# Kernel optimization log

Measured on AMD Instinct MI355X. Metric: run time of the kernel, lower is better.

The kernel has to match this reference:

```python
import jax, jax.numpy as jnp
import numpy as np

N, E, DIN, H, C, ED = 50000, 500000, 264, 4, 32, 16
HID = H * C   # 128
OUT = 128
NEG_SLOPE = 0.2
LN_EPS = 1e-5


def _ln(x, g, b):
    mu = jnp.mean(x, axis=-1, keepdims=True)
    var = jnp.mean((x - mu) ** 2, axis=-1, keepdims=True)
    return (x - mu) * jax.lax.rsqrt(var + LN_EPS) * g + b


def _segment_softmax(scores, seg, num_segments):
    # scores: (E, H), seg: (E,) destination node ids
    m = jax.ops.segment_max(scores, seg, num_segments=num_segments)
    m = jnp.where(jnp.isfinite(m), m, 0.0)
    ex = jnp.exp(scores - m[seg])
    s = jax.ops.segment_sum(ex, seg, num_segments=num_segments)
    return ex / (s[seg] + 1e-16)


def _gatv2(x, src, dst, edge_attr, Wl, bl, Wr, br, We, att, bias):
    # GATv2Conv (PyG semantics): lin_l -> source, lin_r -> target, lin_edge (no bias)
    n = x.shape[0]
    xl = (x @ Wl + bl).reshape(n, H, C)          # source transform
    xr = (x @ Wr + br).reshape(n, H, C)          # target transform
    ee = (edge_attr @ We).reshape(-1, H, C)      # (E, H, C)
    m = xl[src] + xr[dst] + ee                   # per-edge pre-activation
    g = jnp.where(m > 0, m, NEG_SLOPE * m)       # leaky_relu(0.2)
    score = jnp.einsum('ehc,hc->eh', g, att)     # (E, H)
    alpha = _segment_softmax(score, dst, n)      # softmax over in-edges of each dst
    msg = xl[src] * alpha[..., None]             # (E, H, C)
    out = jax.ops.segment_sum(msg, dst, num_segments=n)
    return out.reshape(n, HID) + bias


def setup_inputs() -> dict:
    key = jax.random.key(0)
    ks = jax.random.split(key, 16)
    r = lambda k, s: jax.random.normal(k, s, dtype=jnp.float32) * 0.05
    return {
        'x': jax.random.normal(ks[0], (N, DIN), jnp.float32),
        'edge_attr': jax.random.normal(ks[1], (E, ED), jnp.float32),
        'Wl1': r(ks[2], (DIN, HID)), 'bl1': jnp.zeros((HID,), jnp.float32),
        'Wr1': r(ks[3], (DIN, HID)), 'br1': jnp.zeros((HID,), jnp.float32),
        'We1': r(ks[4], (ED, HID)), 'att1': r(ks[5], (H, C)), 'bias1': jnp.zeros((HID,), jnp.float32),
        'Wl2': r(ks[6], (HID, HID)), 'bl2': jnp.zeros((HID,), jnp.float32),
        'Wr2': r(ks[7], (HID, HID)), 'br2': jnp.zeros((HID,), jnp.float32),
        'We2': r(ks[8], (ED, HID)), 'att2': r(ks[9], (H, C)), 'bias2': jnp.zeros((HID,), jnp.float32),
        'Wres': r(ks[10], (DIN, HID)), 'bres': jnp.zeros((HID,), jnp.float32),
        'Wout': r(ks[11], (HID, OUT)), 'bout': jnp.zeros((OUT,), jnp.float32),
        'g1': jnp.ones((HID,), jnp.float32), 'bn1': jnp.zeros((HID,), jnp.float32),
        'g2': jnp.ones((HID,), jnp.float32), 'bn2': jnp.zeros((HID,), jnp.float32),
        'go': jnp.ones((OUT,), jnp.float32), 'bo': jnp.zeros((OUT,), jnp.float32),
        'edge_index': jax.random.randint(ks[12], (2, E), 0, N, dtype=jnp.int32),
    }


def reference(x, edge_attr, Wl1, bl1, Wr1, br1, We1, att1, bias1,
              Wl2, bl2, Wr2, br2, We2, att2, bias2,
              Wres, bres, Wout, bout, g1, bn1, g2, bn2, go, bo, edge_index):
    src, dst = edge_index[0], edge_index[1]
    residual = x @ Wres + bres
    h = _gatv2(x, src, dst, edge_attr, Wl1, bl1, Wr1, br1, We1, att1, bias1)
    h = jax.nn.elu(h)
    h = _ln(h + residual, g1, bn1)
    residual = h
    h = _gatv2(h, src, dst, edge_attr, Wl2, bl2, Wr2, br2, We2, att2, bias2)
    h = jax.nn.elu(h)
    h = _ln(h + residual, g2, bn2)
    context = _ln(h @ Wout + bout, go, bo)
    return context
```

## Files before the change

kernel.cpp:

```cpp
#include <hip/hip_runtime.h>
#include <hip/hip_bf16.h>
#include <math.h>
#include <stdint.h>

#define NN 50000
#define NE 500000
#define DIN 264
#define KP1 288
#define HID 128
#define EDIM 16

typedef __attribute__((ext_vector_type(8))) short short8;
typedef __attribute__((ext_vector_type(4))) float f32x4;

__device__ __forceinline__ short f2bf(float v) {
    union { float f; unsigned u; } x; x.f = v;
    unsigned r = x.u + 0x7fff + ((x.u >> 16) & 1);
    return (short)(r >> 16);
}
__device__ __forceinline__ float bf2f(short v) {
    union { float f; unsigned u; } x;
    x.u = ((unsigned)(unsigned short)v) << 16;
    return x.f;
}
__device__ __forceinline__ float bflo(unsigned u) {
    union { float f; unsigned u; } x; x.u = u << 16; return x.f;
}
__device__ __forceinline__ float bfhi(unsigned u) {
    union { float f; unsigned u; } x; x.u = u & 0xffff0000u; return x.f;
}
__device__ __forceinline__ unsigned pk2bf(float a, float b) {
    return (unsigned)(unsigned short)f2bf(a) | ((unsigned)(unsigned short)f2bf(b) << 16);
}

__device__ __forceinline__ void gload_lds16(const void* g, void* l) {
    __builtin_amdgcn_global_load_lds(
        (const __attribute__((address_space(1))) unsigned int*)g,
        (__attribute__((address_space(3))) unsigned int*)l, 16, 0, 0);
}

__global__ void k_count(const int* __restrict__ dst, int* __restrict__ cnt) {
    int e = blockIdx.x * blockDim.x + threadIdx.x;
    if (e < NE) atomicAdd(&cnt[dst[e]], 1);
}

__global__ __launch_bounds__(256) void k_scan1(const int* __restrict__ cnt,
                                               int* __restrict__ off, int* __restrict__ bsum) {
    __shared__ int buf[256];
    int b = blockIdx.x, t = threadIdx.x;
    int i = b * 256 + t;
    int v = (i < NN) ? cnt[i] : 0;
    buf[t] = v; __syncthreads();
    for (int s = 1; s < 256; s <<= 1) {
        int u = (t >= s) ? buf[t - s] : 0; __syncthreads();
        buf[t] += u; __syncthreads();
    }
    if (i < NN) off[i + 1] = buf[t];
    if (t == 255) bsum[b] = buf[255];
}

__global__ void k_scan2(int* __restrict__ bsum, int nb) {
    __shared__ int buf[256];
    int t = threadIdx.x;
    int o = (t < nb) ? bsum[t] : 0;
    buf[t] = o; __syncthreads();
    for (int s = 1; s < 256; s <<= 1) {
        int u = (t >= s) ? buf[t - s] : 0; __syncthreads();
        buf[t] += u; __syncthreads();
    }
    if (t < nb) bsum[t] = buf[t] - o;
}

__global__ void k_scan3c(int* __restrict__ off, const int* __restrict__ bsum,
                         int* __restrict__ cur) {
    int j = blockIdx.x * 256 + threadIdx.x;
    if (j > NN) return;
    int v = (j == 0) ? 0 : off[j] + bsum[(j - 1) >> 8];
    off[j] = v;
    if (j < NN) cur[j] = v;
}

__global__ void k_scatter(const int* __restrict__ src, const int* __restrict__ dst,
                          int* __restrict__ cur, int* __restrict__ srcp,
                          int* __restrict__ dstp, int* __restrict__ ey) {
    int e = blockIdx.x * blockDim.x + threadIdx.x;
    if (e < NE) {
        int d = dst[e];
        int p = atomicAdd(&cur[d], 1);
        srcp[p] = src[e];
        dstp[p] = d;
        ey[p] = e;
    }
}

__global__ void k_cvt_x(const float* __restrict__ x, short* __restrict__ xb) {
    int idx = blockIdx.x * 256 + threadIdx.x;
    if (idx >= NN * KP1) return;
    int i = idx / KP1, k = idx - i * KP1;
    xb[idx] = (k < DIN) ? f2bf(x[(size_t)i * DIN + k]) : (short)0;
}

__global__ void k_prep_w(const float* __restrict__ Wl1, const float* __restrict__ Wr1,
                         const float* __restrict__ Wres, const float* __restrict__ Wl2,
                         const float* __restrict__ Wr2, const float* __restrict__ Wout,
                         const float* __restrict__ bl1, const float* __restrict__ br1,
                         const float* __restrict__ bres, const float* __restrict__ bl2,
                         const float* __restrict__ br2,
                         const float* __restrict__ We1, const float* __restrict__ We2,
                         const float* __restrict__ att1, const float* __restrict__ att2,
                         short* __restrict__ Wt1, short* __restrict__ Wt2,
                         short* __restrict__ Wt3, float* __restrict__ bcat1,
                         float* __restrict__ bcat2,
                         short* __restrict__ WeT1, short* __restrict__ WeT2,
                         short* __restrict__ attB1, short* __restrict__ attB2) {
    int idx = blockIdx.x * 256 + threadIdx.x;
    if (idx < 384 * KP1) {
        int n = idx / KP1, k = idx - n * KP1;
        float v = 0.f;
        if (k < DIN) {
            const float* W = (n < 128) ? Wl1 : ((n < 256) ? Wr1 : Wres);
            v = W[(size_t)k * 128 + (n & 127)];
        }
        Wt1[idx] = f2bf(v);
        return;
    }
    idx -= 384 * KP1;
    if (idx < 256 * 128) {
        int n = idx >> 7, k = idx & 127;
        const float* W = (n < 128) ? Wl2 : Wr2;
        Wt2[idx] = f2bf(W[(size_t)k * 128 + (n & 127)]);
        return;
    }
    idx -= 256 * 128;
    if (idx < 128 * 128) {
        int n = idx >> 7, k = idx & 127;
        Wt3[idx] = f2bf(Wout[(size_t)k * 128 + n]);
        return;
    }
    idx -= 128 * 128;
    if (idx < 384) {
        bcat1[idx] = (idx < 128) ? bl1[idx] : ((idx < 256) ? br1[idx - 128] : bres[idx - 256]);
        return;
    }
    idx -= 384;
    if (idx < 256) {
        bcat2[idx] = (idx < 128) ? bl2[idx] : br2[idx - 128];
        return;
    }
    idx -= 256;
    if (idx < 128 * 32) {
        int n = idx >> 5, k = idx & 31;
        WeT1[idx] = (k < EDIM) ? f2bf(We1[(size_t)k * 128 + n]) : (short)0;
        return;
    }
    idx -= 128 * 32;
    if (idx < 128 * 32) {
        int n = idx >> 5, k = idx & 31;
        WeT2[idx] = (k < EDIM) ? f2bf(We2[(size_t)k * 128 + n]) : (short)0;
        return;
    }
    idx -= 128 * 32;
    if (idx < 16 * 128) {
        int n = idx >> 7, k = idx & 127;
        attB1[idx] = (n == (k >> 5)) ? f2bf(att1[k]) : (short)0;
        return;
    }
    idx -= 16 * 128;
    if (idx < 16 * 128) {
        int n = idx >> 7, k = idx & 127;
        attB2[idx] = (n == (k >> 5)) ? f2bf(att2[k]) : (short)0;
    }
}

__global__ __launch_bounds__(256) void k_gather_ea(const int* __restrict__ ey,
                                                   const float* __restrict__ ea,
                                                   short* __restrict__ eaperm) {
    int pos = blockIdx.x * 256 + threadIdx.x;
    if (pos >= NE) return;
    int e = ey[pos];
    const float4* r = (const float4*)(ea + (size_t)e * EDIM);
    float4 v0 = r[0], v1 = r[1], v2 = r[2], v3 = r[3];
    uint4 w0 = make_uint4(pk2bf(v0.x, v0.y), pk2bf(v0.z, v0.w),
                          pk2bf(v1.x, v1.y), pk2bf(v1.z, v1.w));
    uint4 w1 = make_uint4(pk2bf(v2.x, v2.y), pk2bf(v2.z, v2.w),
                          pk2bf(v3.x, v3.y), pk2bf(v3.z, v3.w));
    uint4* o = (uint4*)(eaperm + (size_t)pos * 32);
    o[0] = w0; o[1] = w1;
    o[2] = make_uint4(0, 0, 0, 0);
    o[3] = make_uint4(0, 0, 0, 0);
}

template <bool BF16OUT>
__global__ __launch_bounds__(256) void k_mfma_gemm(const short* __restrict__ A,
                                                   const short* __restrict__ Bt,
                                                   const float* __restrict__ bias,
                                                   float* __restrict__ Cf,
                                                   short* __restrict__ Cb,
                                                   int M, int Kpad, int NS) {
    __shared__ short As[128 * 32];
    __shared__ short Bs[128 * 32];
    int t = threadIdx.x;
    int lane = t & 63, wid = t >> 6;
    int wm = (wid & 1) * 64, wn = (wid >> 1) * 64;
    int cl = lane & 15, quad = lane >> 4;
    int row0 = blockIdx.x * 128;
    int col0 = blockIdx.y * 128;

    f32x4 acc[4][4];
#pragma unroll
    for (int i = 0; i < 4; ++i)
#pragma unroll
        for (int j = 0; j < 4; ++j) acc[i][j] = (f32x4)0.f;

    for (int k0 = 0; k0 < Kpad; k0 += 32) {
#pragma unroll
        for (int r = 0; r < 2; ++r) {
            int c = t + r * 256;
            int m = c >> 2;
            int row = row0 + m; if (row >= M) row = M - 1;
            const char* ga = (const char*)A + ((size_t)row * Kpad + k0) * 2 + (c & 3) * 16;
            gload_lds16(ga, (char*)As + c * 16);
            int n = col0 + m;
            const char* gb = (const char*)Bt + ((size_t)n * Kpad + k0) * 2 + (c & 3) * 16;
            gload_lds16(gb, (char*)Bs + c * 16);
        }
        __syncthreads();

        short8 a[4], b[4];
#pragma unroll
        for (int mi = 0; mi < 4; ++mi)
            a[mi] = *(const short8*)&As[(wm + mi * 16 + cl) * 32 + quad * 8];
#pragma unroll
        for (int ni = 0; ni < 4; ++ni)
            b[ni] = *(const short8*)&Bs[(wn + ni * 16 + cl) * 32 + quad * 8];
#pragma unroll
        for (int mi = 0; mi < 4; ++mi)
#pragma unroll
            for (int ni = 0; ni < 4; ++ni)
                acc[mi][ni] = __builtin_amdgcn_mfma_f32_16x16x32_bf16(a[mi], b[ni], acc[mi][ni], 0, 0, 0);
        __syncthreads();
    }

#pragma unroll
    for (int mi = 0; mi < 4; ++mi)
#pragma unroll
        for (int ni = 0; ni < 4; ++ni) {
            int col = col0 + wn + ni * 16 + cl;
            float bv = bias[col];
#pragma unroll
            for (int r = 0; r < 4; ++r) {
                int row = row0 + wm + mi * 16 + quad * 4 + r;
                if (row < M) {
                    float v = acc[mi][ni][r] + bv;
                    if (BF16OUT) Cb[(size_t)row * NS + col] = f2bf(v);
                    else         Cf[(size_t)row * NS + col] = v;
                }
            }
        }
}

__global__ __launch_bounds__(256) void k_gemm_ln(const short* __restrict__ A,
                                                 const short* __restrict__ Bt,
                                                 const float* __restrict__ bias,
                                                 const float* __restrict__ gamma,
                                                 const float* __restrict__ beta,
                                                 float* __restrict__ out, int M) {
    __shared__ short As[128 * 32];
    __shared__ short Bs[128 * 32];
    __shared__ float redS[128][2];
    int t = threadIdx.x;
    int lane = t & 63, wid = t >> 6;
    int wm = (wid & 1) * 64, wn = (wid >> 1) * 64;
    int cl = lane & 15, quad = lane >> 4;
    int row0 = blockIdx.x * 128;
    int wh = wid >> 1;

    f32x4 acc[4][4];
#pragma unroll
    for (int i = 0; i < 4; ++i)
#pragma unroll
        for (int j = 0; j < 4; ++j) acc[i][j] = (f32x4)0.f;

    for (int k0 = 0; k0 < 128; k0 += 32) {
#pragma unroll
        for (int r = 0; r < 2; ++r) {
            int c = t + r * 256;
            int m = c >> 2;
            int row = row0 + m; if (row >= M) row = M - 1;
            const char* ga = (const char*)A + ((size_t)row * 128 + k0) * 2 + (c & 3) * 16;
            gload_lds16(ga, (char*)As + c * 16);
            const char* gb = (const char*)Bt + ((size_t)m * 128 + k0) * 2 + (c & 3) * 16;
            gload_lds16(gb, (char*)Bs + c * 16);
        }
        __syncthreads();

        short8 a[4], b[4];
#pragma unroll
        for (int mi = 0; mi < 4; ++mi)
            a[mi] = *(const short8*)&As[(wm + mi * 16 + cl) * 32 + quad * 8];
#pragma unroll
        for (int ni = 0; ni < 4; ++ni)
            b[ni] = *(const short8*)&Bs[(wn + ni * 16 + cl) * 32 + quad * 8];
#pragma unroll
        for (int mi = 0; mi < 4; ++mi)
#pragma unroll
            for (int ni = 0; ni < 4; ++ni)
                acc[mi][ni] = __builtin_amdgcn_mfma_f32_16x16x32_bf16(a[mi], b[ni], acc[mi][ni], 0, 0, 0);
        __syncthreads();
    }

    float bv[4], gv[4], bev[4];
#pragma unroll
    for (int ni = 0; ni < 4; ++ni) {
        int col = wn + ni * 16 + cl;
        bv[ni] = bias[col]; gv[ni] = gamma[col]; bev[ni] = beta[col];
    }

    float s[4][4];
#pragma unroll
    for (int mi = 0; mi < 4; ++mi)
#pragma unroll
        for (int r = 0; r < 4; ++r) {
            float v = (acc[mi][0][r] + bv[0]) + (acc[mi][1][r] + bv[1]) +
                      (acc[mi][2][r] + bv[2]) + (acc[mi][3][r] + bv[3]);
            v += __shfl_xor(v, 1, 64);
            v += __shfl_xor(v, 2, 64);
            v += __shfl_xor(v, 4, 64);
            v += __shfl_xor(v, 8, 64);
            s[mi][r] = v;
        }
    if (cl == 0) {
#pragma unroll
        for (int mi = 0; mi < 4; ++mi)
#pragma unroll
            for (int r = 0; r < 4; ++r)
                redS[wm + mi * 16 + quad * 4 + r][wh] = s[mi][r];
    }
    __syncthreads();
    float mean[4][4];
#pragma unroll
    for (int mi = 0; mi < 4; ++mi)
#pragma unroll
        for (int r = 0; r < 4; ++r) {
            int rl = wm + mi * 16 + quad * 4 + r;
            mean[mi][r] = (redS[rl][0] + redS[rl][1]) * (1.f / 128.f);
        }
    __syncthreads();

#pragma unroll
    for (int mi = 0; mi < 4; ++mi)
#pragma unroll
        for (int r = 0; r < 4; ++r) {
            float q = 0.f;
#pragma unroll
            for (int ni = 0; ni < 4; ++ni) {
                float d = acc[mi][ni][r] + bv[ni] - mean[mi][r];
                q = fmaf(d, d, q);
            }
            q += __shfl_xor(q, 1, 64);
            q += __shfl_xor(q, 2, 64);
            q += __shfl_xor(q, 4, 64);
            q += __shfl_xor(q, 8, 64);
            s[mi][r] = q;
        }
    if (cl == 0) {
#pragma unroll
        for (int mi = 0; mi < 4; ++mi)
#pragma unroll
            for (int r = 0; r < 4; ++r)
                redS[wm + mi * 16 + quad * 4 + r][wh] = s[mi][r];
    }
    __syncthreads();

#pragma unroll
    for (int mi = 0; mi < 4; ++mi)
#pragma unroll
        for (int r = 0; r < 4; ++r) {
            int rl = wm + mi * 16 + quad * 4 + r;
            int row = row0 + rl;
            if (row < M) {
                float rstd = rsqrtf((redS[rl][0] + redS[rl][1]) * (1.f / 128.f) + 1e-5f);
#pragma unroll
                for (int ni = 0; ni < 4; ++ni) {
                    int col = wn + ni * 16 + cl;
                    float d = acc[mi][ni][r] + bv[ni] - mean[mi][r];
                    out[(size_t)row * 128 + col] = fmaf(d * rstd, gv[ni], bev[ni]);
                }
            }
        }
}

template <int STRIDE>
__global__ __launch_bounds__(512) void k_edge_score(const short* __restrict__ eaperm,
                                                    const short* __restrict__ WeT,
                                                    const short* __restrict__ attB,
                                                    const int* __restrict__ srcp,
                                                    const int* __restrict__ dstp,
                                                    const short* __restrict__ C,
                                                    float* __restrict__ pe) {
    __shared__ short Gs[128 * 136];
    __shared__ short Ab[16 * 136];
    __shared__ int sS[128], sD[128];
    int t = threadIdx.x;
    int lane = t & 63, wid = t >> 6;
    int wm2 = (wid & 1) * 64;
    int wn2 = (wid >> 1) * 32;
    int cl = lane & 15, quad = lane >> 4;
    long e0 = (long)blockIdx.x * 128;

    if (t < 128) {
        long ep = e0 + t; if (ep >= NE) ep = NE - 1;
        sS[t] = srcp[ep];
        sD[t] = dstp[ep];
    } else if (t < 384) {
        int u = t - 128;
        int rr = u >> 4, cc = (u & 15) * 8;
        *(short8*)&Ab[rr * 136 + cc] = *(const short8*)&attB[rr * 128 + cc];
    }

    short8 a[4], b[2];
#pragma unroll
    for (int mi = 0; mi < 4; ++mi) {
        long e = e0 + wm2 + mi * 16 + cl; if (e >= NE) e = NE - 1;
        a[mi] = *(const short8*)&eaperm[e * 32 + quad * 8];
    }
#pragma unroll
    for (int ni = 0; ni < 2; ++ni)
        b[ni] = *(const short8*)&WeT[(size_t)(wn2 + ni * 16 + cl) * 32 + quad * 8];

    f32x4 acc[4][2];
#pragma unroll
    for (int i = 0; i < 4; ++i) { acc[i][0] = (f32x4)0.f; acc[i][1] = (f32x4)0.f; }
#pragma unroll
    for (int mi = 0; mi < 4; ++mi)
#pragma unroll
        for (int ni = 0; ni < 2; ++ni)
            acc[mi][ni] = __builtin_amdgcn_mfma_f32_16x16x32_bf16(a[mi], b[ni], acc[mi][ni], 0, 0, 0);
    __syncthreads();

#pragma unroll
    for (int mi = 0; mi < 4; ++mi) {
#pragma unroll
        for (int r = 0; r < 4; ++r) {
            int eloc = wm2 + mi * 16 + quad * 4 + r;
            const short* xlr = C + (size_t)sS[eloc] * STRIDE;
            const short* xrr = C + (size_t)sD[eloc] * STRIDE + 128;
            int f0 = wn2 + cl, f1 = wn2 + 16 + cl;
            float xl0 = bf2f(xlr[f0]), xr0 = bf2f(xrr[f0]);
            float xl1 = bf2f(xlr[f1]), xr1 = bf2f(xrr[f1]);
            float g0 = acc[mi][0][r] + xl0 + xr0;
            float g1 = acc[mi][1][r] + xl1 + xr1;
            g0 = fmaxf(g0, 0.2f * g0);
            g1 = fmaxf(g1, 0.2f * g1);
            Gs[eloc * 136 + f0] = f2bf(g0);
            Gs[eloc * 136 + f1] = f2bf(g1);
        }
    }
    __syncthreads();

    f32x4 sacc = (f32x4)0.f;
    int em0 = wid * 16;
#pragma unroll
    for (int ks = 0; ks < 4; ++ks) {
        short8 ag = *(const short8*)&Gs[(em0 + cl) * 136 + ks * 32 + quad * 8];
        short8 bg = *(const short8*)&Ab[cl * 136 + ks * 32 + quad * 8];
        sacc = __builtin_amdgcn_mfma_f32_16x16x32_bf16(ag, bg, sacc, 0, 0, 0);
    }

    if (cl < 4) {
#pragma unroll
        for (int r = 0; r < 4; ++r) {
            long epos = e0 + em0 + quad * 4 + r;
            if (epos < NE) pe[epos * 4 + cl] = __expf(sacc[r]);
        }
    }
}

template <int STRIDE>
__global__ __launch_bounds__(256) void k_fused_agg(const int* __restrict__ off,
                                                   const int* __restrict__ srcp,
                                                   const float* __restrict__ pe,
                                                   const short* __restrict__ C,
                                                   const short* __restrict__ resid, int rstride,
                                                   const float* __restrict__ bias,
                                                   const float* __restrict__ gamma,
                                                   const float* __restrict__ beta,
                                                   short* __restrict__ outb) {
    int t = threadIdx.x;
    int w = t >> 6, l = t & 63;
    int f0 = (l >> 4) * 32 + (l & 15) * 2;
    int fp = f0 >> 1;
    int hd = l >> 4;

    float2 bs2 = ((const float2*)bias)[fp];
    float2 gv = ((const float2*)gamma)[fp];
    float2 bev = ((const float2*)beta)[fp];

    int n0 = (blockIdx.x * 4 + w) * 4;
    int nend = n0 + 4; if (nend > NN) nend = NN;

    for (int i = n0; i < nend; ++i) {
        unsigned rp = *(const unsigned*)&resid[(size_t)i * rstride + f0];
        int b0 = off[i], b1 = off[i + 1];

        float lA = 0.f, aA0 = 0.f, aA1 = 0.f;
        float lB = 0.f, aB0 = 0.f, aB1 = 0.f;
        int pos = b0;
        int sA = 0, sB = 0; float pA = 0.f, pB = 0.f;
        bool have = (pos + 2 <= b1);
        if (have) {
            sA = srcp[pos]; sB = srcp[pos + 1];
            pA = pe[(size_t)pos * 4 + hd]; pB = pe[(size_t)(pos + 1) * 4 + hd];
        }
        while (have) {
            bool haven = (pos + 4 <= b1);
            int nsA = 0, nsB = 0; float npA = 0.f, npB = 0.f;
            if (haven) {
                nsA = srcp[pos + 2]; nsB = srcp[pos + 3];
                npA = pe[(size_t)(pos + 2) * 4 + hd]; npB = pe[(size_t)(pos + 3) * 4 + hd];
            }
            unsigned xlA = *(const unsigned*)&C[(size_t)sA * STRIDE + f0];
            unsigned xlB = *(const unsigned*)&C[(size_t)sB * STRIDE + f0];
            lA += pA; lB += pB;
            aA0 = fmaf(pA, bflo(xlA), aA0);
            aA1 = fmaf(pA, bfhi(xlA), aA1);
            aB0 = fmaf(pB, bflo(xlB), aB0);
            aB1 = fmaf(pB, bfhi(xlB), aB1);
            pos += 2;
            sA = nsA; sB = nsB; pA = npA; pB = npB;
            have = haven;
        }
        if (pos < b1) {
            int s1 = srcp[pos];
            float p1 = pe[(size_t)pos * 4 + hd];
            unsigned xlv = *(const unsigned*)&C[(size_t)s1 * STRIDE + f0];
            lA += p1;
            aA0 = fmaf(p1, bflo(xlv), aA0);
            aA1 = fmaf(p1, bfhi(xlv), aA1);
        }
        float l_run = lA + lB;
        float acc0 = aA0 + aB0, acc1 = aA1 + aB1;

        float inv = 1.f / (l_run + 1e-16f);
        float o0 = fmaf(acc0, inv, bs2.x);
        float o1 = fmaf(acc1, inv, bs2.y);
        o0 = o0 > 0.f ? o0 : (__expf(o0) - 1.f);
        o1 = o1 > 0.f ? o1 : (__expf(o1) - 1.f);
        float v0 = o0 + bflo(rp), v1 = o1 + bfhi(rp);
        float s = v0 + v1;
#pragma unroll
        for (int o = 32; o > 0; o >>= 1) s += __shfl_xor(s, o, 64);
        float mean = s * (1.f / 128.f);
        float d0 = v0 - mean, d1 = v1 - mean;
        float q = fmaf(d0, d0, d1 * d1);
#pragma unroll
        for (int o = 32; o > 0; o >>= 1) q += __shfl_xor(q, o, 64);
        float rstd = rsqrtf(q * (1.f / 128.f) + 1e-5f);
        float r0 = fmaf(d0 * rstd, gv.x, bev.x);
        float r1 = fmaf(d1 * rstd, gv.y, bev.y);
        unsigned op = (unsigned)(unsigned short)f2bf(r0) |
                      (((unsigned)(unsigned short)f2bf(r1)) << 16);
        *(unsigned*)&outb[(size_t)i * 128 + f0] = op;
    }
}

extern "C" void kernel_launch(void* const* d_in, const int* in_sizes, int n_in,
                              void* d_out, int out_size, void* d_ws, size_t ws_size,
                              hipStream_t stream) {
    (void)in_sizes; (void)n_in; (void)out_size; (void)ws_size;
    const float* x     = (const float*)d_in[0];
    const float* ea    = (const float*)d_in[1];
    const float* Wl1   = (const float*)d_in[2];
    const float* bl1   = (const float*)d_in[3];
    const float* Wr1   = (const float*)d_in[4];
    const float* br1   = (const float*)d_in[5];
    const float* We1   = (const float*)d_in[6];
    const float* att1  = (const float*)d_in[7];
    const float* bias1 = (const float*)d_in[8];
    const float* Wl2   = (const float*)d_in[9];
    const float* bl2   = (const float*)d_in[10];
    const float* Wr2   = (const float*)d_in[11];
    const float* br2   = (const float*)d_in[12];
    const float* We2   = (const float*)d_in[13];
    const float* att2  = (const float*)d_in[14];
    const float* bias2 = (const float*)d_in[15];
    const float* Wres  = (const float*)d_in[16];
    const float* bres  = (const float*)d_in[17];
    const float* Wout  = (const float*)d_in[18];
    const float* bout  = (const float*)d_in[19];
    const float* g1    = (const float*)d_in[20];
    const float* bn1   = (const float*)d_in[21];
    const float* g2    = (const float*)d_in[22];
    const float* bn2   = (const float*)d_in[23];
    const float* go    = (const float*)d_in[24];
    const float* bo    = (const float*)d_in[25];
    const int*   ei    = (const int*)d_in[26];
    const int* srcv = ei;
    const int* dstv = ei + NE;
    float* outp = (float*)d_out;

    char* p = (char*)d_ws;
    auto carve = [&](size_t bytes) {
        char* r = p;
        p += (bytes + 255) & ~(size_t)255;
        return r;
    };
    short* xb    = (short*)carve((size_t)NN * KP1 * 2);
    short* Wt1   = (short*)carve((size_t)384 * KP1 * 2);
    short* Wt2   = (short*)carve((size_t)256 * 128 * 2);
    short* Wt3   = (short*)carve((size_t)128 * 128 * 2);
    short* WeT1  = (short*)carve((size_t)128 * 32 * 2);
    short* WeT2  = (short*)carve((size_t)128 * 32 * 2);
    short* attB1 = (short*)carve((size_t)16 * 128 * 2);
    short* attB2 = (short*)carve((size_t)16 * 128 * 2);
    float* bcat1 = (float*)carve(384 * 4);
    float* bcat2 = (float*)carve(256 * 4);
    short* C1    = (short*)carve((size_t)NN * 384 * 2);
    short* h1b   = (short*)carve((size_t)NN * 128 * 2);
    short* h2b   = (short*)carve((size_t)NN * 128 * 2);
    int* off     = (int*)carve((size_t)(NN + 1) * 4);
    int* cur     = (int*)carve((size_t)NN * 4);
    int* bsum    = (int*)carve(256 * 4);
    int* srcp    = (int*)carve((size_t)NE * 4);
    int* dstp    = (int*)carve((size_t)NE * 4);
    int* ey      = (int*)carve((size_t)NE * 4);
    short* eaperm = (short*)carve((size_t)NE * 32 * 2);
    float* pe    = (float*)carve((size_t)NE * 4 * 4);

    short* C2 = C1;

    const int NB = (NN + 255) / 256;

    hipMemsetAsync(cur, 0, (size_t)NN * 4, stream);
    k_count<<<(NE + 255) / 256, 256, 0, stream>>>(dstv, cur);
    k_scan1<<<NB, 256, 0, stream>>>(cur, off, bsum);
    k_scan2<<<1, 256, 0, stream>>>(bsum, NB);
    k_scan3c<<<(NN + 256) / 256, 256, 0, stream>>>(off, bsum, cur);
    k_scatter<<<(NE + 255) / 256, 256, 0, stream>>>(srcv, dstv, cur, srcp, dstp, ey);

    k_cvt_x<<<((size_t)NN * KP1 + 255) / 256, 256, 0, stream>>>(x, xb);
    int prep_total = 384 * KP1 + 256 * 128 + 128 * 128 + 384 + 256 + 2 * 128 * 32 + 2 * 16 * 128;
    k_prep_w<<<(prep_total + 255) / 256, 256, 0, stream>>>(Wl1, Wr1, Wres, Wl2, Wr2, Wout,
                                                           bl1, br1, bres, bl2, br2,
                                                           We1, We2, att1, att2,
                                                           Wt1, Wt2, Wt3, bcat1, bcat2,
                                                           WeT1, WeT2, attB1, attB2);
    k_gather_ea<<<(NE + 255) / 256, 256, 0, stream>>>(ey, ea, eaperm);

    int mb  = (NN + 127) / 128;
    int ebk = (NE + 127) / 128;
    int gagg = (NN + 15) / 16;

    k_mfma_gemm<true><<<dim3(mb, 3), 256, 0, stream>>>(xb, Wt1, bcat1, nullptr, C1, NN, KP1, 384);
    k_edge_score<384><<<ebk, 512, 0, stream>>>(eaperm, WeT1, attB1, srcp, dstp, C1, pe);
    k_fused_agg<384><<<gagg, 256, 0, stream>>>(off, srcp, pe, C1,
                                               C1 + 256, 384, bias1, g1, bn1, h1b);
    k_mfma_gemm<true><<<dim3(mb, 2), 256, 0, stream>>>(h1b, Wt2, bcat2, nullptr, C2, NN, 128, 256);
    k_edge_score<256><<<ebk, 512, 0, stream>>>(eaperm, WeT2, attB2, srcp, dstp, C2, pe);
    k_fused_agg<256><<<gagg, 256, 0, stream>>>(off, srcp, pe, C2,
                                               h1b, 128, bias2, g2, bn2, h2b);
    k_gemm_ln<<<mb, 256, 0, stream>>>(h2b, Wt3, bout, go, bo, outp, NN);
}
```

Before: 483.8 us.

## Drop permuted edge-attr buffer; gather and convert edge attributes inside edge-score kernel

```diff
diff --git a/kernel.cpp b/kernel.cpp
--- a/kernel.cpp
+++ b/kernel.cpp
@@ -28,9 +28,6 @@
 }
 __device__ __forceinline__ float bfhi(unsigned u) {
     union { float f; unsigned u; } x; x.u = u & 0xffff0000u; return x.f;
-}
-__device__ __forceinline__ unsigned pk2bf(float a, float b) {
-    return (unsigned)(unsigned short)f2bf(a) | ((unsigned)(unsigned short)f2bf(b) << 16);
 }
 
 __device__ __forceinline__ void gload_lds16(const void* g, void* l) {
@@ -81,15 +78,20 @@
 }
 
 __global__ void k_scatter(const int* __restrict__ src, const int* __restrict__ dst,
-                          int* __restrict__ cur, int* __restrict__ srcp,
-                          int* __restrict__ dstp, int* __restrict__ ey) {
+                          int* __restrict__ cur, int2* __restrict__ csr_se) {
     int e = blockIdx.x * blockDim.x + threadIdx.x;
     if (e < NE) {
         int d = dst[e];
         int p = atomicAdd(&cur[d], 1);
-        srcp[p] = src[e];
-        dstp[p] = d;
-        ey[p] = e;
+        csr_se[p] = make_int2(src[e], e);
+    }
+}
+
+__global__ void k_fill_dst(const int* __restrict__ off, int* __restrict__ dstp) {
+    int i = blockIdx.x * 256 + threadIdx.x;
+    if (i < NN) {
+        int b0 = off[i], b1 = off[i + 1];
+        for (int p = b0; p < b1; ++p) dstp[p] = i;
     }
 }
 
@@ -172,24 +174,6 @@
     }
 }
 
-__global__ __launch_bounds__(256) void k_gather_ea(const int* __restrict__ ey,
-                                                   const float* __restrict__ ea,
-                                                   short* __restrict__ eaperm) {
-    int pos = blockIdx.x * 256 + threadIdx.x;
-    if (pos >= NE) return;
-    int e = ey[pos];
-    const float4* r = (const float4*)(ea + (size_t)e * EDIM);
-    float4 v0 = r[0], v1 = r[1], v2 = r[2], v3 = r[3];
-    uint4 w0 = make_uint4(pk2bf(v0.x, v0.y), pk2bf(v0.z, v0.w),
-                          pk2bf(v1.x, v1.y), pk2bf(v1.z, v1.w));
-    uint4 w1 = make_uint4(pk2bf(v2.x, v2.y), pk2bf(v2.z, v2.w),
-                          pk2bf(v3.x, v3.y), pk2bf(v3.z, v3.w));
-    uint4* o = (uint4*)(eaperm + (size_t)pos * 32);
-    o[0] = w0; o[1] = w1;
-    o[2] = make_uint4(0, 0, 0, 0);
-    o[3] = make_uint4(0, 0, 0, 0);
-}
-
 template <bool BF16OUT>
 __global__ __launch_bounds__(256) void k_mfma_gemm(const short* __restrict__ A,
                                                    const short* __restrict__ Bt,
@@ -391,11 +375,11 @@
 }
 
 template <int STRIDE>
-__global__ __launch_bounds__(512) void k_edge_score(const short* __restrict__ eaperm,
+__global__ __launch_bounds__(512) void k_edge_score(const int2* __restrict__ csr_se,
+                                                    const int* __restrict__ dstp,
+                                                    const float* __restrict__ ea,
                                                     const short* __restrict__ WeT,
                                                     const short* __restrict__ attB,
-                                                    const int* __restrict__ srcp,
-                                                    const int* __restrict__ dstp,
                                                     const short* __restrict__ C,
                                                     float* __restrict__ pe) {
     __shared__ short Gs[128 * 136];
@@ -410,7 +394,7 @@
 
     if (t < 128) {
         long ep = e0 + t; if (ep >= NE) ep = NE - 1;
-        sS[t] = srcp[ep];
+        sS[t] = csr_se[ep].x;
         sD[t] = dstp[ep];
     } else if (t < 384) {
         int u = t - 128;
@@ -422,7 +406,17 @@
 #pragma unroll
     for (int mi = 0; mi < 4; ++mi) {
         long e = e0 + wm2 + mi * 16 + cl; if (e >= NE) e = NE - 1;
-        a[mi] = *(const short8*)&eaperm[e * 32 + quad * 8];
+        if (quad < 2) {
+            int eid = csr_se[e].y;
+            const float4* r = (const float4*)(ea + (size_t)eid * EDIM + quad * 8);
+            float4 v0 = r[0], v1 = r[1];
+            short8 av;
+            av[0] = f2bf(v0.x); av[1] = f2bf(v0.y); av[2] = f2bf(v0.z); av[3] = f2bf(v0.w);
+            av[4] = f2bf(v1.x); av[5] = f2bf(v1.y); av[6] = f2bf(v1.z); av[7] = f2bf(v1.w);
+            a[mi] = av;
+        } else {
+            a[mi] = (short8)0;
+        }
     }
 #pragma unroll
     for (int ni = 0; ni < 2; ++ni)
@@ -478,7 +472,7 @@
 
 template <int STRIDE>
 __global__ __launch_bounds__(256) void k_fused_agg(const int* __restrict__ off,
-                                                   const int* __restrict__ srcp,
+                                                   const int2* __restrict__ csr_se,
                                                    const float* __restrict__ pe,
                                                    const short* __restrict__ C,
                                                    const short* __restrict__ resid, int rstride,
@@ -509,14 +503,14 @@
         int sA = 0, sB = 0; float pA = 0.f, pB = 0.f;
         bool have = (pos + 2 <= b1);
         if (have) {
-            sA = srcp[pos]; sB = srcp[pos + 1];
+            sA = csr_se[pos].x; sB = csr_se[pos + 1].x;
             pA = pe[(size_t)pos * 4 + hd]; pB = pe[(size_t)(pos + 1) * 4 + hd];
         }
         while (have) {
             bool haven = (pos + 4 <= b1);
             int nsA = 0, nsB = 0; float npA = 0.f, npB = 0.f;
             if (haven) {
-                nsA = srcp[pos + 2]; nsB = srcp[pos + 3];
+                nsA = csr_se[pos + 2].x; nsB = csr_se[pos + 3].x;
                 npA = pe[(size_t)(pos + 2) * 4 + hd]; npB = pe[(size_t)(pos + 3) * 4 + hd];
             }
             unsigned xlA = *(const unsigned*)&C[(size_t)sA * STRIDE + f0];
@@ -531,7 +525,7 @@
             have = haven;
         }
         if (pos < b1) {
-            int s1 = srcp[pos];
+            int s1 = csr_se[pos].x;
             float p1 = pe[(size_t)pos * 4 + hd];
             unsigned xlv = *(const unsigned*)&C[(size_t)s1 * STRIDE + f0];
             lA += p1;
@@ -621,10 +615,8 @@
     int* off     = (int*)carve((size_t)(NN + 1) * 4);
     int* cur     = (int*)carve((size_t)NN * 4);
     int* bsum    = (int*)carve(256 * 4);
-    int* srcp    = (int*)carve((size_t)NE * 4);
+    int2* csr_se = (int2*)carve((size_t)NE * 8);
     int* dstp    = (int*)carve((size_t)NE * 4);
-    int* ey      = (int*)carve((size_t)NE * 4);
-    short* eaperm = (short*)carve((size_t)NE * 32 * 2);
     float* pe    = (float*)carve((size_t)NE * 4 * 4);
 
     short* C2 = C1;
@@ -636,7 +628,8 @@
     k_scan1<<<NB, 256, 0, stream>>>(cur, off, bsum);
     k_scan2<<<1, 256, 0, stream>>>(bsum, NB);
     k_scan3c<<<(NN + 256) / 256, 256, 0, stream>>>(off, bsum, cur);
-    k_scatter<<<(NE + 255) / 256, 256, 0, stream>>>(srcv, dstv, cur, srcp, dstp, ey);
+    k_scatter<<<(NE + 255) / 256, 256, 0, stream>>>(srcv, dstv, cur, csr_se);
+    k_fill_dst<<<NB, 256, 0, stream>>>(off, dstp);
 
     k_cvt_x<<<((size_t)NN * KP1 + 255) / 256, 256, 0, stream>>>(x, xb);
     int prep_total = 384 * KP1 + 256 * 128 + 128 * 128 + 384 + 256 + 2 * 128 * 32 + 2 * 16 * 128;
@@ -645,19 +638,18 @@
                                                            We1, We2, att1, att2,
                                                            Wt1, Wt2, Wt3, bcat1, bcat2,
                                                            WeT1, WeT2, attB1, attB2);
-    k_gather_ea<<<(NE + 255) / 256, 256, 0, stream>>>(ey, ea, eaperm);
 
     int mb  = (NN + 127) / 128;
     int ebk = (NE + 127) / 128;
     int gagg = (NN + 15) / 16;
 
     k_mfma_gemm<true><<<dim3(mb, 3), 256, 0, stream>>>(xb, Wt1, bcat1, nullptr, C1, NN, KP1, 384);
-    k_edge_score<384><<<ebk, 512, 0, stream>>>(eaperm, WeT1, attB1, srcp, dstp, C1, pe);
-    k_fused_agg<384><<<gagg, 256, 0, stream>>>(off, srcp, pe, C1,
+    k_edge_score<384><<<ebk, 512, 0, stream>>>(csr_se, dstp, ea, WeT1, attB1, C1, pe);
+    k_fused_agg<384><<<gagg, 256, 0, stream>>>(off, csr_se, pe, C1,
                                                C1 + 256, 384, bias1, g1, bn1, h1b);
     k_mfma_gemm<true><<<dim3(mb, 2), 256, 0, stream>>>(h1b, Wt2, bcat2, nullptr, C2, NN, 128, 256);
-    k_edge_score<256><<<ebk, 512, 0, stream>>>(eaperm, WeT2, attB2, srcp, dstp, C2, pe);
-    k_fused_agg<256><<<gagg, 256, 0, stream>>>(off, srcp, pe, C2,
+    k_edge_score<256><<<ebk, 512, 0, stream>>>(csr_se, dstp, ea, WeT2, attB2, C2, pe);
+    k_fused_agg<256><<<gagg, 256, 0, stream>>>(off, csr_se, pe, C2,
                                                h1b, 128, bias2, g2, bn2, h2b);
     k_gemm_ln<<<mb, 256, 0, stream>>>(h2b, Wt3, bout, go, bo, outp, NN);
 }
```

Measured after the change: 488.3 us. About the same (+0.9%).
